# Kernel optimization log

Hardware: AMD Instinct MI355X
Metric: run time of the kernel (lower is better)

The kernel has to match this reference:

```python
import jax, jax.numpy as jnp
import numpy as np

DIM = 768
HEADS = 12
DIM_HEAD = DIM // HEADS
FACTOR = DIM_HEAD ** (-0.5)
B, T = 4, 2048


def setup_inputs() -> dict:
    key = jax.random.key(0)
    k1, k2, k3 = jax.random.split(key, 3)
    x = jax.random.normal(k1, (B, T, DIM), dtype=jnp.float32)
    # VarianceScaling-like init scale for linear weights
    W_qkv = jax.random.normal(k2, (DIM, 3 * DIM), dtype=jnp.float32) * (DIM ** -0.5)
    W_out = jax.random.normal(k3, (DIM, DIM), dtype=jnp.float32) * (DIM ** -0.5)
    return {"x": x, "W_qkv": W_qkv, "W_out": W_out}


def reference(x, W_qkv, W_out):
    b, t, _ = x.shape
    qkv = x @ W_qkv  # [b, t, 3*dim]
    # einops 'b t (d k h) -> k b h t d' with k=3, h=HEADS: d slowest, k middle, h fastest
    qkv = qkv.reshape(b, t, DIM_HEAD, 3, HEADS)
    qkv = jnp.transpose(qkv, (3, 0, 4, 1, 2))  # [3, b, h, t, d]
    q, k, v = qkv[0], qkv[1], qkv[2]
    # scaled dot-product attention, full [b,h,t,t] scores as in the original
    scores = jnp.einsum('bhid,bhjd->bhij', q, k) * FACTOR
    attn = jax.nn.softmax(scores, axis=-1)
    out = jnp.einsum('bhij,bhjd->bhid', attn, v)  # [b, h, t, d]
    # 'b h t d -> b t (h d)'
    out = jnp.transpose(out, (0, 2, 1, 3)).reshape(b, t, HEADS * DIM_HEAD)
    return out @ W_out
```

## Files before the change

### kernel.cpp

```cpp
#include <hip/hip_runtime.h>
#include <hip/hip_bf16.h>

#define DIM    768
#define HEADS  12
#define DHEAD  64
#define BATCH  4
#define SEQ    2048
#define NROW   (BATCH * SEQ)
#define QKVN   (3 * DIM)
#define FACTOR 0.125f
#define QSCALE 0.18033688011112042f

typedef __attribute__((ext_vector_type(8))) short short8;
typedef __attribute__((ext_vector_type(4))) float floatx4;
typedef __attribute__((ext_vector_type(16))) float floatx16;
typedef __attribute__((ext_vector_type(4))) unsigned uintx4;

__device__ __forceinline__ floatx4 mfma16(short8 a, short8 b, floatx4 c) {
    return __builtin_amdgcn_mfma_f32_16x16x32_bf16(a, b, c, 0, 0, 0);
}
__device__ __forceinline__ floatx16 mfma32(short8 a, short8 b, floatx16 c) {
    return __builtin_amdgcn_mfma_f32_32x32x16_bf16(a, b, c, 0, 0, 0);
}

__device__ __forceinline__ void glds16(const void* g, void* l) {
    __builtin_amdgcn_global_load_lds((const __attribute__((address_space(1))) void*)g,
                                     (__attribute__((address_space(3))) void*)l,
                                     16, 0, 0);
}

__device__ __forceinline__ short rne16(float f) {
    unsigned u = __builtin_bit_cast(unsigned, f);
    return (short)((u + 0x7fffu + ((u >> 16) & 1u)) >> 16);
}
__device__ __forceinline__ unsigned pack2(float lo, float hi) {
    unsigned ul = __builtin_bit_cast(unsigned, lo);
    unsigned uh = __builtin_bit_cast(unsigned, hi);
    ul = (ul + 0x7fffu + ((ul >> 16) & 1u)) >> 16;
    uh = (uh + 0x7fffu + ((uh >> 16) & 1u)) & 0xffff0000u;
    return ul | uh;
}
__device__ __forceinline__ unsigned cvtpk(float lo, float hi) {
    unsigned r;
    asm("v_cvt_pk_bf16_f32 %0, %1, %2" : "=v"(r) : "v"(lo), "v"(hi));
    return r;
}

__device__ __forceinline__ int swz8(int row, int col) {
    return (row << 6) + ((((col >> 3) ^ row) & 7) << 3) + (col & 7);
}

__global__ __launch_bounds__(256) void prep(const float* __restrict__ x,
                                            short* __restrict__ xb,
                                            const float* __restrict__ Wqkv,
                                            short* __restrict__ Wqt,
                                            const float* __restrict__ Wout,
                                            short* __restrict__ Wot) {
    __shared__ short T[32][33];
    int blk = blockIdx.x;
    if (blk < 6144) {
        int g = blk * 256 + threadIdx.x;
        float4 v = ((const float4*)x)[g];
        uint2 o;
        o.x = pack2(v.x, v.y);
        o.y = pack2(v.z, v.w);
        ((uint2*)xb)[g] = o;
        return;
    }
    blk -= 6144;
    const float* W;
    short* Wt;
    int N, permute, bx, by;
    if (blk < 1728) { W = Wqkv; Wt = Wqt; N = QKVN; permute = 1; bx = blk % 72; by = blk / 72; }
    else { blk -= 1728; W = Wout; Wt = Wot; N = DIM; permute = 0; bx = blk % 24; by = blk / 24; }

    int n0 = bx * 32, k0 = by * 32;
    int c = threadIdx.x & 31, r0 = threadIdx.x >> 5;
    for (int r = r0; r < 32; r += 8)
        T[r][c] = rne16(W[(size_t)(k0 + r) * N + n0 + c]);
    __syncthreads();
    for (int r = r0; r < 32; r += 8) {
        int n = n0 + r;
        int np = n;
        float scale = 1.0f;
        if (permute) {
            int d = n / 36, rem = n - d * 36;
            int which = rem / 12, h = rem - which * 12;
            np = which * 768 + h * 64 + d;
            if (which == 0) scale = QSCALE;
        }
        float v = __bfloat162float(__hip_bfloat16_raw{(unsigned short)T[c][r]});
        Wt[(size_t)np * DIM + k0 + c] = (scale == 1.0f) ? T[c][r] : rne16(v * scale);
    }
}

__global__ __launch_bounds__(256) void gemm_qkv(const short* __restrict__ A,
                                                const short* __restrict__ Bt,
                                                short* __restrict__ Qo,
                                                short* __restrict__ Ko,
                                                short* __restrict__ Vto) {
    __shared__ short As[128 * 64];
    __shared__ short Bs[128 * 64];
    const int tid = threadIdx.x;
    const int lane = tid & 63, wave = tid >> 6;
    const int l15 = lane & 15, quad = lane >> 4;

    const int flat = blockIdx.x;
    const int xcd = flat & 7;
    const int local = flat >> 3;
    const int mloc = local & 7, nloc = local >> 3;
    const int m0 = (xcd * 8 + mloc) * 128;
    const int n0 = nloc * 128;

    const int wm = (wave >> 1) * 64, wn = (wave & 1) * 64;
    const int r8 = wave * 8 + (lane >> 3);
    const int c8 = lane & 7;
    const int sc = ((c8 ^ (r8 & 7)) << 3);

    const int sn = n0 + wn;
    const int which = sn / 768;
    const bool swapAB = (which != 2);

    floatx4 acc[4][4] = {};
    for (int k0 = 0; k0 < DIM; k0 += 64) {
#pragma unroll
        for (int i = 0; i < 4; ++i) {
            int row = i * 32 + r8;
            glds16(&A[(size_t)(m0 + row) * DIM + k0 + sc], &As[(size_t)(i * 32 + wave * 8) * 64]);
            glds16(&Bt[(size_t)(n0 + row) * DIM + k0 + sc], &Bs[(size_t)(i * 32 + wave * 8) * 64]);
        }
        __syncthreads();
#pragma unroll
        for (int ks = 0; ks < 2; ++ks) {
            short8 a[4], b[4];
#pragma unroll
            for (int mt = 0; mt < 4; ++mt)
                a[mt] = *(const short8*)&As[swz8(wm + mt * 16 + l15, ks * 32 + quad * 8)];
#pragma unroll
            for (int nt = 0; nt < 4; ++nt)
                b[nt] = *(const short8*)&Bs[swz8(wn + nt * 16 + l15, ks * 32 + quad * 8)];
            if (swapAB) {
#pragma unroll
                for (int mt = 0; mt < 4; ++mt)
#pragma unroll
                    for (int nt = 0; nt < 4; ++nt)
                        acc[mt][nt] = mfma16(b[nt], a[mt], acc[mt][nt]);
            } else {
#pragma unroll
                for (int mt = 0; mt < 4; ++mt)
#pragma unroll
                    for (int nt = 0; nt < 4; ++nt)
                        acc[mt][nt] = mfma16(a[mt], b[nt], acc[mt][nt]);
            }
        }
        __syncthreads();
    }

    const int h = (sn - which * 768) >> 6;
    const int bb = (m0 + wm) >> 11;

    if (which != 2) {
        const bool isQ = (which == 0);
        short* dst = isQ ? Qo : Ko;
        const size_t tb = isQ
            ? ((size_t)(bb * HEADS + h) * 16 + ((m0 & 2047) >> 7)) * 8192
            : ((size_t)(bb * HEADS + h) * 32 + (((m0 + wm) & 2047) >> 6)) * 4096;
#pragma unroll
        for (int mt = 0; mt < 4; ++mt)
#pragma unroll
            for (int nt = 0; nt < 4; ++nt) {
                int cl = (mt & 1) * 16 + l15 + 32 * (quad >> 1);
                int off = isQ
                    ? (((wm >> 5) + (mt >> 1)) * 2048 + nt * 512 + cl * 8 + (quad & 1) * 4)
                    : (((mt >> 1) * 4 + nt) * 512 + cl * 8 + (quad & 1) * 4);
                uint2 pk;
                pk.x = pack2(acc[mt][nt][0], acc[mt][nt][1]);
                pk.y = pack2(acc[mt][nt][2], acc[mt][nt][3]);
                *(uint2*)&dst[tb + off] = pk;
            }
    } else {
        const size_t tb = ((size_t)(bb * HEADS + h) * 32 + (((m0 + wm) & 2047) >> 6)) * 4096;
#pragma unroll
        for (int mt = 0; mt < 4; ++mt)
#pragma unroll
            for (int nt = 0; nt < 4; ++nt) {
                int cl = (nt & 1) * 16 + l15 + 32 * (quad >> 1);
                int off = ((nt >> 1) * 4 + mt) * 512 + cl * 8 + (quad & 1) * 4;
                uint2 pk;
                pk.x = pack2(acc[mt][nt][0], acc[mt][nt][1]);
                pk.y = pack2(acc[mt][nt][2], acc[mt][nt][3]);
                *(uint2*)&Vto[tb + off] = pk;
            }
    }
}

__global__ __launch_bounds__(256, 3) void attn_mfma(const short* __restrict__ Q,
                                                    const short* __restrict__ K,
                                                    const short* __restrict__ Vt,
                                                    short* __restrict__ O) {
    __shared__ __align__(16) short smem[16384];
    const int tid = threadIdx.x;
    const int lane = tid & 63, wave = tid >> 6;
    const int l31 = lane & 31, hi = lane >> 5;
    const int flat = blockIdx.x;
    const int xcd = flat & 7, li = flat >> 3;
    const int bh = xcd + (li % 6) * 8;
    const int q0 = (li / 6) * 128;
    const size_t base = (size_t)bh * SEQ * DHEAD;
    const int lane8 = lane * 8;

    {
        size_t qtb = base + (size_t)(q0 >> 7) * 8192;
#pragma unroll
        for (int c = 0; c < 4; ++c) {
            int s = wave * 4 + c;
            glds16(&Q[qtb + s * 512 + lane8], &smem[s * 512]);
        }
    }
    __syncthreads();
    short8 qf[4];
#pragma unroll
    for (int ks = 0; ks < 4; ++ks)
        qf[ks] = *(const short8*)&smem[wave * 2048 + ks * 512 + lane8];
    __syncthreads();

    floatx16 o0 = {}, o1 = {};
    float lsum = 0.f;

    glds16(&K[base + (2 * wave + 0) * 512 + lane8], &smem[(2 * wave + 0) * 512]);
    glds16(&K[base + (2 * wave + 1) * 512 + lane8], &smem[(2 * wave + 1) * 512]);
    glds16(&Vt[base + (2 * wave + 0) * 512 + lane8], &smem[4096 + (2 * wave + 0) * 512]);
    glds16(&Vt[base + (2 * wave + 1) * 512 + lane8], &smem[4096 + (2 * wave + 1) * 512]);

    for (int t = 0; t < 32; ++t) {
        __syncthreads();
        const short* Ks = smem + (t & 1) * 8192;
        const short* Vs = Ks + 4096;
        if (t < 31) {
            size_t ktb = base + (size_t)(t + 1) * 4096;
            short* nb = smem + ((t + 1) & 1) * 8192;
            glds16(&K[ktb + (2 * wave + 0) * 512 + lane8], &nb[(2 * wave + 0) * 512]);
            glds16(&K[ktb + (2 * wave + 1) * 512 + lane8], &nb[(2 * wave + 1) * 512]);
            glds16(&Vt[ktb + (2 * wave + 0) * 512 + lane8], &nb[4096 + (2 * wave + 0) * 512]);
            glds16(&Vt[ktb + (2 * wave + 1) * 512 + lane8], &nb[4096 + (2 * wave + 1) * 512]);
        }

        floatx16 sa0 = {}, sa1 = {};
        __builtin_amdgcn_s_setprio(1);
#pragma unroll
        for (int ks = 0; ks < 4; ++ks) {
            short8 kf0 = *(const short8*)&Ks[(0 * 4 + ks) * 512 + lane8];
            short8 kf1 = *(const short8*)&Ks[(1 * 4 + ks) * 512 + lane8];
            sa0 = mfma32(kf0, qf[ks], sa0);
            sa1 = mfma32(kf1, qf[ks], sa1);
        }
        __builtin_amdgcn_s_setprio(0);

        short8 pf[4];
#define SOFTPACK(SA, PFA, PFB) {                                              \
        float e0_  = __builtin_amdgcn_exp2f(SA[0]);                           \
        float e1_  = __builtin_amdgcn_exp2f(SA[1]);                           \
        float e2_  = __builtin_amdgcn_exp2f(SA[2]);                           \
        float e3_  = __builtin_amdgcn_exp2f(SA[3]);                           \
        float e4_  = __builtin_amdgcn_exp2f(SA[4]);                           \
        float e5_  = __builtin_amdgcn_exp2f(SA[5]);                           \
        float e6_  = __builtin_amdgcn_exp2f(SA[6]);                           \
        float e7_  = __builtin_amdgcn_exp2f(SA[7]);                           \
        float e8_  = __builtin_amdgcn_exp2f(SA[8]);                           \
        float e9_  = __builtin_amdgcn_exp2f(SA[9]);                           \
        float e10_ = __builtin_amdgcn_exp2f(SA[10]);                          \
        float e11_ = __builtin_amdgcn_exp2f(SA[11]);                          \
        float e12_ = __builtin_amdgcn_exp2f(SA[12]);                          \
        float e13_ = __builtin_amdgcn_exp2f(SA[13]);                          \
        float e14_ = __builtin_amdgcn_exp2f(SA[14]);                          \
        float e15_ = __builtin_amdgcn_exp2f(SA[15]);                          \
        lsum += (((e0_ + e1_) + (e2_ + e3_)) + ((e4_ + e5_) + (e6_ + e7_)))   \
              + (((e8_ + e9_) + (e10_ + e11_)) + ((e12_ + e13_) + (e14_ + e15_))); \
        unsigned A0_ = cvtpk(e0_, e1_),   A1_ = cvtpk(e2_, e3_);              \
        unsigned B0_ = cvtpk(e4_, e5_),   B1_ = cvtpk(e6_, e7_);              \
        unsigned C0_ = cvtpk(e8_, e9_),   C1_ = cvtpk(e10_, e11_);            \
        unsigned E0_ = cvtpk(e12_, e13_), E1_ = cvtpk(e14_, e15_);            \
        asm("v_permlane32_swap_b32 %0, %1" : "+v"(A0_), "+v"(B0_));           \
        asm("v_permlane32_swap_b32 %0, %1" : "+v"(A1_), "+v"(B1_));           \
        asm("v_permlane32_swap_b32 %0, %1" : "+v"(C0_), "+v"(E0_));           \
        asm("v_permlane32_swap_b32 %0, %1" : "+v"(C1_), "+v"(E1_));           \
        uintx4 wa_ = {A0_, A1_, B0_, B1_};                                    \
        uintx4 wb_ = {C0_, C1_, E0_, E1_};                                    \
        PFA = __builtin_bit_cast(short8, wa_);                                \
        PFB = __builtin_bit_cast(short8, wb_);                                \
    }
        SOFTPACK(sa0, pf[0], pf[1])
        SOFTPACK(sa1, pf[2], pf[3])
#undef SOFTPACK

        __builtin_amdgcn_s_setprio(1);
#pragma unroll
        for (int kc = 0; kc < 4; ++kc) {
            short8 vf0 = *(const short8*)&Vs[(0 * 4 + kc) * 512 + lane8];
            short8 vf1 = *(const short8*)&Vs[(1 * 4 + kc) * 512 + lane8];
            o0 = mfma32(vf0, pf[kc], o0);
            o1 = mfma32(vf1, pf[kc], o1);
        }
        __builtin_amdgcn_s_setprio(0);
    }

    float s = lsum + __shfl_xor(lsum, 32);
    float inv = 1.f / s;

    const int b = bh / HEADS, h = bh - b * HEADS;
    const int tq = q0 + wave * 32 + l31;
    size_t rowo = ((size_t)(b * SEQ + tq)) * DIM + h * DHEAD;
#pragma unroll
    for (int blk = 0; blk < 4; ++blk) {
        int d0 = 8 * blk + 4 * hi;
        uint2 p0, p1;
        p0.x = cvtpk(o0[4 * blk + 0] * inv, o0[4 * blk + 1] * inv);
        p0.y = cvtpk(o0[4 * blk + 2] * inv, o0[4 * blk + 3] * inv);
        *(uint2*)&O[rowo + d0] = p0;
        p1.x = cvtpk(o1[4 * blk + 0] * inv, o1[4 * blk + 1] * inv);
        p1.y = cvtpk(o1[4 * blk + 2] * inv, o1[4 * blk + 3] * inv);
        *(uint2*)&O[rowo + 32 + d0] = p1;
    }
}

__global__ __launch_bounds__(256) void gemm_out(const short* __restrict__ A,
                                                const short* __restrict__ Bt,
                                                float* __restrict__ out) {
    __shared__ short As[128 * 64];
    __shared__ short Bs[128 * 64];
    const int tid = threadIdx.x;
    const int lane = tid & 63, wave = tid >> 6;
    const int l15 = lane & 15, quad = lane >> 4;
    const int m0 = blockIdx.y * 128, n0 = blockIdx.x * 128;
    const int wm = (wave >> 1) * 64, wn = (wave & 1) * 64;
    const int r8 = wave * 8 + (lane >> 3);
    const int sc = (((lane & 7) ^ (r8 & 7)) << 3);

    floatx4 acc[4][4] = {};
    for (int k0 = 0; k0 < DIM; k0 += 64) {
#pragma unroll
        for (int i = 0; i < 4; ++i) {
            int row = i * 32 + r8;
            glds16(&A[(size_t)(m0 + row) * DIM + k0 + sc], &As[(size_t)(i * 32 + wave * 8) * 64]);
            glds16(&Bt[(size_t)(n0 + row) * DIM + k0 + sc], &Bs[(size_t)(i * 32 + wave * 8) * 64]);
        }
        __syncthreads();
#pragma unroll
        for (int ks = 0; ks < 2; ++ks) {
            short8 a[4], b[4];
#pragma unroll
            for (int mt = 0; mt < 4; ++mt)
                a[mt] = *(const short8*)&As[swz8(wm + mt * 16 + l15, ks * 32 + quad * 8)];
#pragma unroll
            for (int nt = 0; nt < 4; ++nt)
                b[nt] = *(const short8*)&Bs[swz8(wn + nt * 16 + l15, ks * 32 + quad * 8)];
#pragma unroll
            for (int mt = 0; mt < 4; ++mt)
#pragma unroll
                for (int nt = 0; nt < 4; ++nt)
                    acc[mt][nt] = mfma16(b[nt], a[mt], acc[mt][nt]);
        }
        __syncthreads();
    }

#pragma unroll
    for (int mt = 0; mt < 4; ++mt)
#pragma unroll
        for (int nt = 0; nt < 4; ++nt) {
            int m = m0 + wm + mt * 16 + l15;
            int n = n0 + wn + nt * 16 + quad * 4;
            *(floatx4*)&out[(size_t)m * DIM + n] = acc[mt][nt];
        }
}

extern "C" void kernel_launch(void* const* d_in, const int* in_sizes, int n_in,
                              void* d_out, int out_size, void* d_ws, size_t ws_size,
                              hipStream_t stream) {
    const float* x    = (const float*)d_in[0];
    const float* Wqkv = (const float*)d_in[1];
    const float* Wout = (const float*)d_in[2];
    float* out = (float*)d_out;

    const size_t NE = (size_t)NROW * DIM;
    short* xb  = (short*)d_ws;
    short* Wqt = xb + NE;
    short* Wot = Wqt + (size_t)QKVN * DIM;
    short* Qw  = Wot + (size_t)DIM * DIM;
    short* Kw  = Qw + NE;
    short* Vtw = Kw + NE;

    prep<<<6144 + 1728 + 576, 256, 0, stream>>>(x, xb, Wqkv, Wqt, Wout, Wot);
    gemm_qkv<<<8 * 8 * 18, 256, 0, stream>>>(xb, Wqt, Qw, Kw, Vtw);
    attn_mfma<<<768, 256, 0, stream>>>(Qw, Kw, Vtw, xb);
    gemm_out<<<dim3(DIM / 128, NROW / 128), 256, 0, stream>>>(xb, Wot, out);
}
```

Baseline: 210.1 us.

## Software-pipeline attention QK and PV across tiles; shrink out-GEMM M tile

The attention loop moves to a triple-buffered K/V ring so that QK^T for the current tile is issued alongside PV for the previous tile's probabilities. This lets softmax exp/pack overlap with MFMA work from another stage. Separately, the output GEMM tile drops from 128x128 to 64x128, doubling the number of blocks so the 768-wide output fills more CUs. The cost is more LDS per attention block (48KB), which may reduce occupancy at 3 blocks/CU, plus extra registers to hold the carried probabilities.

After: 207.5 us. Within noise of the previous version (-1.2%).

```diff
diff --git a/kernel.cpp b/kernel.cpp
--- a/kernel.cpp
+++ b/kernel.cpp
@@ -198,7 +198,7 @@
                                                     const short* __restrict__ K,
                                                     const short* __restrict__ Vt,
                                                     short* __restrict__ O) {
-    __shared__ __align__(16) short smem[16384];
+    __shared__ __align__(16) short smem[24576];
     const int tid = threadIdx.x;
     const int lane = tid & 63, wave = tid >> 6;
     const int l31 = lane & 31, hi = lane >> 5;
@@ -227,36 +227,17 @@
     floatx16 o0 = {}, o1 = {};
     float lsum = 0.f;
 
-    glds16(&K[base + (2 * wave + 0) * 512 + lane8], &smem[(2 * wave + 0) * 512]);
-    glds16(&K[base + (2 * wave + 1) * 512 + lane8], &smem[(2 * wave + 1) * 512]);
-    glds16(&Vt[base + (2 * wave + 0) * 512 + lane8], &smem[4096 + (2 * wave + 0) * 512]);
-    glds16(&Vt[base + (2 * wave + 1) * 512 + lane8], &smem[4096 + (2 * wave + 1) * 512]);
-
-    for (int t = 0; t < 32; ++t) {
-        __syncthreads();
-        const short* Ks = smem + (t & 1) * 8192;
-        const short* Vs = Ks + 4096;
-        if (t < 31) {
-            size_t ktb = base + (size_t)(t + 1) * 4096;
-            short* nb = smem + ((t + 1) & 1) * 8192;
-            glds16(&K[ktb + (2 * wave + 0) * 512 + lane8], &nb[(2 * wave + 0) * 512]);
-            glds16(&K[ktb + (2 * wave + 1) * 512 + lane8], &nb[(2 * wave + 1) * 512]);
-            glds16(&Vt[ktb + (2 * wave + 0) * 512 + lane8], &nb[4096 + (2 * wave + 0) * 512]);
-            glds16(&Vt[ktb + (2 * wave + 1) * 512 + lane8], &nb[4096 + (2 * wave + 1) * 512]);
-        }
-
-        floatx16 sa0 = {}, sa1 = {};
-        __builtin_amdgcn_s_setprio(1);
-#pragma unroll
-        for (int ks = 0; ks < 4; ++ks) {
-            short8 kf0 = *(const short8*)&Ks[(0 * 4 + ks) * 512 + lane8];
-            short8 kf1 = *(const short8*)&Ks[(1 * 4 + ks) * 512 + lane8];
-            sa0 = mfma32(kf0, qf[ks], sa0);
-            sa1 = mfma32(kf1, qf[ks], sa1);
-        }
-        __builtin_amdgcn_s_setprio(0);
-
-        short8 pf[4];
+    const int seg0 = (2 * wave + 0) * 512;
+    const int seg1 = (2 * wave + 1) * 512;
+
+#define STAGE(tt, buf) {                                                \
+        size_t ktb_ = base + (size_t)(tt) * 4096;                       \
+        glds16(&K[ktb_ + seg0 + lane8], &(buf)[seg0]);                  \
+        glds16(&K[ktb_ + seg1 + lane8], &(buf)[seg1]);                  \
+        glds16(&Vt[ktb_ + seg0 + lane8], &(buf)[4096 + seg0]);          \
+        glds16(&Vt[ktb_ + seg1 + lane8], &(buf)[4096 + seg1]);          \
+    }
+
 #define SOFTPACK(SA, PFA, PFB) {                                              \
         float e0_  = __builtin_amdgcn_exp2f(SA[0]);                           \
         float e1_  = __builtin_amdgcn_exp2f(SA[1]);                           \
@@ -289,20 +270,69 @@
         PFA = __builtin_bit_cast(short8, wa_);                                \
         PFB = __builtin_bit_cast(short8, wb_);                                \
     }
-        SOFTPACK(sa0, pf[0], pf[1])
-        SOFTPACK(sa1, pf[2], pf[3])
+
+#define QK(Ks, SA0, SA1) {                                                    \
+        __builtin_amdgcn_s_setprio(1);                                        \
+        _Pragma("unroll")                                                     \
+        for (int ks_ = 0; ks_ < 4; ++ks_) {                                   \
+            short8 kf0_ = *(const short8*)&(Ks)[(0 * 4 + ks_) * 512 + lane8]; \
+            short8 kf1_ = *(const short8*)&(Ks)[(1 * 4 + ks_) * 512 + lane8]; \
+            SA0 = mfma32(kf0_, qf[ks_], SA0);                                 \
+            SA1 = mfma32(kf1_, qf[ks_], SA1);                                 \
+        }                                                                     \
+        __builtin_amdgcn_s_setprio(0);                                        \
+    }
+
+#define PV(Vs, PF) {                                                          \
+        __builtin_amdgcn_s_setprio(1);                                        \
+        _Pragma("unroll")                                                     \
+        for (int kc_ = 0; kc_ < 4; ++kc_) {                                   \
+            short8 vf0_ = *(const short8*)&(Vs)[(0 * 4 + kc_) * 512 + lane8]; \
+            short8 vf1_ = *(const short8*)&(Vs)[(1 * 4 + kc_) * 512 + lane8]; \
+            o0 = mfma32(vf0_, PF[kc_], o0);                                   \
+            o1 = mfma32(vf1_, PF[kc_], o1);                                   \
+        }                                                                     \
+        __builtin_amdgcn_s_setprio(0);                                        \
+    }
+
+    short8 pfp[4];
+
+    STAGE(0, smem);
+    {
+        __syncthreads();
+        STAGE(1, smem + 8192);
+        floatx16 sa0 = {}, sa1 = {};
+        QK(smem, sa0, sa1);
+        SOFTPACK(sa0, pfp[0], pfp[1])
+        SOFTPACK(sa1, pfp[2], pfp[3])
+    }
+
+    int bp = 0, bc = 1, bn = 2;
+    for (int t = 1; t < 32; ++t) {
+        __syncthreads();
+        short* curb = smem + bc * 8192;
+        short* prvb = smem + bp * 8192;
+        if (t < 31)
+            STAGE(t + 1, smem + bn * 8192);
+
+        floatx16 sa0 = {}, sa1 = {};
+        QK(curb, sa0, sa1);
+        PV(prvb + 4096, pfp);
+
+        short8 pfc[4];
+        SOFTPACK(sa0, pfc[0], pfc[1])
+        SOFTPACK(sa1, pfc[2], pfc[3])
+#pragma unroll
+        for (int i = 0; i < 4; ++i) pfp[i] = pfc[i];
+
+        bp = bc; bc = bn; bn = (bn == 2) ? 0 : bn + 1;
+    }
+    PV(smem + bp * 8192 + 4096, pfp);
+
+#undef QK
+#undef PV
 #undef SOFTPACK
-
-        __builtin_amdgcn_s_setprio(1);
-#pragma unroll
-        for (int kc = 0; kc < 4; ++kc) {
-            short8 vf0 = *(const short8*)&Vs[(0 * 4 + kc) * 512 + lane8];
-            short8 vf1 = *(const short8*)&Vs[(1 * 4 + kc) * 512 + lane8];
-            o0 = mfma32(vf0, pf[kc], o0);
-            o1 = mfma32(vf1, pf[kc], o1);
-        }
-        __builtin_amdgcn_s_setprio(0);
-    }
+#undef STAGE
 
     float s = lsum + __shfl_xor(lsum, 32);
     float inv = 1.f / s;
@@ -326,38 +356,42 @@
 __global__ __launch_bounds__(256) void gemm_out(const short* __restrict__ A,
                                                 const short* __restrict__ Bt,
                                                 float* __restrict__ out) {
-    __shared__ short As[128 * 64];
+    __shared__ short As[64 * 64];
     __shared__ short Bs[128 * 64];
     const int tid = threadIdx.x;
     const int lane = tid & 63, wave = tid >> 6;
     const int l15 = lane & 15, quad = lane >> 4;
-    const int m0 = blockIdx.y * 128, n0 = blockIdx.x * 128;
-    const int wm = (wave >> 1) * 64, wn = (wave & 1) * 64;
+    const int m0 = blockIdx.y * 64, n0 = blockIdx.x * 128;
+    const int wn = wave * 32;
     const int r8 = wave * 8 + (lane >> 3);
     const int sc = (((lane & 7) ^ (r8 & 7)) << 3);
 
-    floatx4 acc[4][4] = {};
+    floatx4 acc[4][2] = {};
     for (int k0 = 0; k0 < DIM; k0 += 64) {
+#pragma unroll
+        for (int i = 0; i < 2; ++i) {
+            int row = i * 32 + r8;
+            glds16(&A[(size_t)(m0 + row) * DIM + k0 + sc], &As[(size_t)(i * 32 + wave * 8) * 64]);
+        }
 #pragma unroll
         for (int i = 0; i < 4; ++i) {
             int row = i * 32 + r8;
-            glds16(&A[(size_t)(m0 + row) * DIM + k0 + sc], &As[(size_t)(i * 32 + wave * 8) * 64]);
             glds16(&Bt[(size_t)(n0 + row) * DIM + k0 + sc], &Bs[(size_t)(i * 32 + wave * 8) * 64]);
         }
         __syncthreads();
 #pragma unroll
         for (int ks = 0; ks < 2; ++ks) {
-            short8 a[4], b[4];
+            short8 a[4], b[2];
 #pragma unroll
             for (int mt = 0; mt < 4; ++mt)
-                a[mt] = *(const short8*)&As[swz8(wm + mt * 16 + l15, ks * 32 + quad * 8)];
-#pragma unroll
-            for (int nt = 0; nt < 4; ++nt)
+                a[mt] = *(const short8*)&As[swz8(mt * 16 + l15, ks * 32 + quad * 8)];
+#pragma unroll
+            for (int nt = 0; nt < 2; ++nt)
                 b[nt] = *(const short8*)&Bs[swz8(wn + nt * 16 + l15, ks * 32 + quad * 8)];
 #pragma unroll
             for (int mt = 0; mt < 4; ++mt)
 #pragma unroll
-                for (int nt = 0; nt < 4; ++nt)
+                for (int nt = 0; nt < 2; ++nt)
                     acc[mt][nt] = mfma16(b[nt], a[mt], acc[mt][nt]);
         }
         __syncthreads();
@@ -366,8 +400,8 @@
 #pragma unroll
     for (int mt = 0; mt < 4; ++mt)
 #pragma unroll
-        for (int nt = 0; nt < 4; ++nt) {
-            int m = m0 + wm + mt * 16 + l15;
+        for (int nt = 0; nt < 2; ++nt) {
+            int m = m0 + mt * 16 + l15;
             int n = n0 + wn + nt * 16 + quad * 4;
             *(floatx4*)&out[(size_t)m * DIM + n] = acc[mt][nt];
         }
@@ -392,5 +426,5 @@
     prep<<<6144 + 1728 + 576, 256, 0, stream>>>(x, xb, Wqkv, Wqt, Wout, Wot);
     gemm_qkv<<<8 * 8 * 18, 256, 0, stream>>>(xb, Wqt, Qw, Kw, Vtw);
     attn_mfma<<<768, 256, 0, stream>>>(Qw, Kw, Vtw, xb);
-    gemm_out<<<dim3(DIM / 128, NROW / 128), 256, 0, stream>>>(xb, Wot, out);
-}
+    gemm_out<<<dim3(DIM / 128, NROW / 64), 256, 0, stream>>>(xb, Wot, out);
+}
```
